# Performance work log

Hardware: AMD Instinct MI355X
Metric: run time of the kernel (lower is better)

## Reference

```python
import jax, jax.numpy as jnp
import numpy as np


def _bilinear_sample(tex, grid):
    """grid_sample, bilinear, align_corners=True, padding_mode='zeros'.
    tex: [C, Hin, Win]; grid: [B, Ho, Wo, 2] in [-1, 1] (x=width, y=height).
    Returns [B, C, Ho, Wo].
    """
    C, Hin, Win = tex.shape
    gx, gy = grid[..., 0], grid[..., 1]
    # align_corners=True mapping
    ix = (gx + 1.0) * 0.5 * (Win - 1)
    iy = (gy + 1.0) * 0.5 * (Hin - 1)
    ix0 = jnp.floor(ix)
    iy0 = jnp.floor(iy)
    wx1 = ix - ix0
    wy1 = iy - iy0
    wx0 = 1.0 - wx1
    wy0 = 1.0 - wy1

    def gather(iy_, ix_):
        valid = (ix_ >= 0) & (ix_ <= Win - 1) & (iy_ >= 0) & (iy_ <= Hin - 1)
        ic = jnp.clip(ix_, 0, Win - 1).astype(jnp.int32)
        jc = jnp.clip(iy_, 0, Hin - 1).astype(jnp.int32)
        v = tex[:, jc, ic]  # [C, B, Ho, Wo]
        return v * valid.astype(tex.dtype)[None]

    out = (gather(iy0, ix0) * (wy0 * wx0)[None]
           + gather(iy0, ix0 + 1) * (wy0 * wx1)[None]
           + gather(iy0 + 1, ix0) * (wy1 * wx0)[None]
           + gather(iy0 + 1, ix0 + 1) * (wy1 * wx1)[None])
    return jnp.transpose(out, (1, 0, 2, 3))  # [B, C, Ho, Wo]


def setup_inputs() -> dict:
    key = jax.random.key(0)
    k = jax.random.split(key, 6)
    B, C, W, H = 4, 16, 1024, 1024
    Ho, Wo = 512, 512
    return {
        "x": jax.random.uniform(k[0], (B, Ho, Wo, 2), dtype=jnp.float32),
        "x_msk": jax.random.uniform(k[1], (B, Ho, Wo), dtype=jnp.float32),
        "layer1": jax.random.normal(k[2], (C, W, H), dtype=jnp.float32),
        "layer2": jax.random.normal(k[3], (C, W // 2, H // 2), dtype=jnp.float32),
        "layer3": jax.random.normal(k[4], (C, W // 4, H // 4), dtype=jnp.float32),
        "layer4": jax.random.normal(k[5], (C, W // 8, H // 8), dtype=jnp.float32),
    }


def reference(x, x_msk, layer1, layer2, layer3, layer4):
    grid = x * 2.0 - 1.0
    y = (_bilinear_sample(layer1, grid)
         + _bilinear_sample(layer2, grid)
         + _bilinear_sample(layer3, grid)
         + _bilinear_sample(layer4, grid))
    return y * x_msk[:, None]
```

## Files before the change

kernel.cpp:

```cpp
#include <hip/hip_runtime.h>
#include <hip/hip_fp16.h>

#define CH 16
#define NPIX (4 * 512 * 512)
#define NBINS 4096
#define NBLK_SORT 256
#define PPB (NPIX / NBLK_SORT)
#define NILV 2720

typedef float vfloat4 __attribute__((ext_vector_type(4)));

__device__ __forceinline__ int bin_of(float xv, float yv) {
  int bx = min(max((int)(xv * 1023.0f), 0), 1023) >> 4;
  int by = min(max((int)(yv * 1023.0f), 0), 1023) >> 4;
  return (by << 6) + bx;
}

__global__ __launch_bounds__(256) void ilv_hist_kernel(
    const float* __restrict__ l1, const float* __restrict__ l2,
    const float* __restrict__ l3, const float* __restrict__ l4,
    __half* __restrict__ w1, __half* __restrict__ w2,
    __half* __restrict__ w3, __half* __restrict__ w4,
    const float2* __restrict__ x, unsigned* __restrict__ hist) {
  __shared__ unsigned s_lds[CH * 258];
  int b = blockIdx.x, t = threadIdx.x;
  if (b >= NILV) {
    int blk = b - NILV;
#pragma unroll
    for (int i = 0; i < NBINS / 256; ++i) s_lds[i * 256 + t] = 0;
    __syncthreads();
    int base = blk * PPB;
#pragma unroll 4
    for (int c = 0; c < PPB / 256; ++c) {
      float2 g = x[base + c * 256 + t];
      atomicAdd(&s_lds[bin_of(g.x, g.y)], 1u);
    }
    __syncthreads();
#pragma unroll
    for (int i = 0; i < NBINS / 256; ++i)
      hist[(size_t)blk * NBINS + i * 256 + t] = s_lds[i * 256 + t];
    return;
  }
  const float* src; __half* dst; int HW; size_t tb;
  if (b < 2048)      { src = l1; dst = w1; HW = 1048576; tb = (size_t)b * 512; }
  else if (b < 2560) { src = l2; dst = w2; HW = 262144;  tb = (size_t)(b - 2048) * 512; }
  else if (b < 2688) { src = l3; dst = w3; HW = 65536;   tb = (size_t)(b - 2560) * 512; }
  else               { src = l4; dst = w4; HW = 16384;   tb = (size_t)(b - 2688) * 512; }
  int lane = t & 63, cg = t >> 6;
#pragma unroll
  for (int j = 0; j < 4; ++j) {
    int c = cg * 4 + j;
    const vfloat4* s4 = (const vfloat4*)(src + (size_t)c * HW + tb);
#pragma unroll
    for (int half_ = 0; half_ < 2; ++half_) {
      vfloat4 v = __builtin_nontemporal_load(&s4[half_ * 64 + lane]);
      unsigned h0 = __half_as_ushort(__float2half(v.x));
      unsigned h1 = __half_as_ushort(__float2half(v.y));
      unsigned h2 = __half_as_ushort(__float2half(v.z));
      unsigned h3 = __half_as_ushort(__float2half(v.w));
      s_lds[c * 258 + half_ * 128 + lane * 2 + 0] = h0 | (h1 << 16);
      s_lds[c * 258 + half_ * 128 + lane * 2 + 1] = h2 | (h3 << 16);
    }
  }
  __syncthreads();
#pragma unroll
  for (int q = 0; q < 2; ++q) {
    int tt = t + q * 256;
    int idx = tt >> 1, sh = (tt & 1) * 16;
    unsigned o[8];
#pragma unroll
    for (int k = 0; k < 8; ++k) {
      unsigned lo = (s_lds[(2 * k + 0) * 258 + idx] >> sh) & 0xffffu;
      unsigned hi = (s_lds[(2 * k + 1) * 258 + idx] >> sh) & 0xffffu;
      o[k] = lo | (hi << 16);
    }
    uint4* d = (uint4*)(dst + (tb + tt) * CH);
    d[0] = make_uint4(o[0], o[1], o[2], o[3]);
    d[1] = make_uint4(o[4], o[5], o[6], o[7]);
  }
}

__global__ __launch_bounds__(256) void colscan2_kernel(
    unsigned* __restrict__ hist, unsigned* __restrict__ totals) {
  int bin = blockIdx.x * 256 + threadIdx.x;
  unsigned run = 0;
  for (int k = 0; k < NBLK_SORT; ++k) {
    size_t idx = (size_t)k * NBINS + bin;
    unsigned v = hist[idx];
    hist[idx] = run;
    run += v;
  }
  totals[bin] = run;
}

__global__ __launch_bounds__(1024) void scan_kernel(
    const unsigned* __restrict__ counts, unsigned* __restrict__ cursor) {
  __shared__ unsigned part[1024];
  int t = threadIdx.x;
  unsigned c0 = counts[4 * t + 0], c1 = counts[4 * t + 1];
  unsigned c2 = counts[4 * t + 2], c3 = counts[4 * t + 3];
  part[t] = c0 + c1 + c2 + c3;
  __syncthreads();
  for (int off = 1; off < 1024; off <<= 1) {
    unsigned v = (t >= off) ? part[t - off] : 0u;
    __syncthreads();
    part[t] += v;
    __syncthreads();
  }
  unsigned base = (t > 0) ? part[t - 1] : 0u;
  cursor[4 * t + 0] = base;
  cursor[4 * t + 1] = base + c0;
  cursor[4 * t + 2] = base + c0 + c1;
  cursor[4 * t + 3] = base + c0 + c1 + c2;
}

__global__ __launch_bounds__(256) void scatter2_kernel(
    const float2* __restrict__ x, const float* __restrict__ msk,
    const unsigned* __restrict__ hist, const unsigned* __restrict__ binbase,
    float4* __restrict__ pixrec) {
  __shared__ unsigned cur[NBINS];
  int tid = threadIdx.x, blk = blockIdx.x;
#pragma unroll
  for (int i = 0; i < NBINS / 256; ++i)
    cur[i * 256 + tid] = hist[(size_t)blk * NBINS + i * 256 + tid] +
                         binbase[i * 256 + tid];
  __syncthreads();
  int base = blk * PPB;
#pragma unroll 4
  for (int c = 0; c < PPB / 256; ++c) {
    int p = base + c * 256 + tid;
    float2 g = x[p];
    float m = msk[p];
    unsigned i = atomicAdd(&cur[bin_of(g.x, g.y)], 1u);
    pixrec[i] = make_float4(g.x, g.y, __uint_as_float((unsigned)p), m);
  }
}

__device__ __forceinline__ void sample_layer(const uint4* __restrict__ base,
                                             int W, float u, float v, int h,
                                             float c00, float c01, float c10,
                                             float c11, float acc[8]) {
  float ix = u * (float)(W - 1);
  float iy = v * (float)(W - 1);
  float fx = floorf(ix), fy = floorf(iy);
  float wx1 = ix - fx, wy1 = iy - fy;
  float wx0 = 1.0f - wx1, wy0 = 1.0f - wy1;
  int x0 = min(max((int)fx, 0), W - 1);
  int x1 = min(x0 + 1, W - 1);
  int y0 = min(max((int)fy, 0), W - 1);
  int y1 = min(y0 + 1, W - 1);
  union { uint4 u4; __half2 hh[4]; } a00, a01, a10, a11;
  a00.u4 = base[((size_t)y0 * W + x0) * 2 + h];
  a01.u4 = base[((size_t)y0 * W + x1) * 2 + h];
  a10.u4 = base[((size_t)y1 * W + x0) * 2 + h];
  a11.u4 = base[((size_t)y1 * W + x1) * 2 + h];
  __half2 w00h = __float2half2_rn(wy0 * wx0 * c00);
  __half2 w01h = __float2half2_rn(wy0 * wx1 * c01);
  __half2 w10h = __float2half2_rn(wy1 * wx0 * c10);
  __half2 w11h = __float2half2_rn(wy1 * wx1 * c11);
#pragma unroll
  for (int i = 0; i < 4; ++i) {
    __half2 s = __hmul2(a00.hh[i], w00h);
    s = __hfma2(a01.hh[i], w01h, s);
    s = __hfma2(a10.hh[i], w10h, s);
    s = __hfma2(a11.hh[i], w11h, s);
    float2 f = __half22float2(s);
    acc[2 * i + 0] += f.x;
    acc[2 * i + 1] += f.y;
  }
}

__global__ __launch_bounds__(256) void gather_binned4_kernel(
    const float4* __restrict__ pixrec,
    const __half* __restrict__ t1, const __half* __restrict__ t2,
    const __half* __restrict__ t3, const __half* __restrict__ t4,
    __half* __restrict__ ws2) {
  __shared__ float4 srec[128];
  __shared__ unsigned qcnt[16];
  __shared__ unsigned qb[16];
  __shared__ unsigned char perm[128];
  int tid = threadIdx.x;
  int bid = blockIdx.x;
  int swz = (bid & 7) * 1024 + (bid >> 3);
  int base = swz * 128;
  if (tid < 16) qcnt[tid] = 0;
  __syncthreads();
  unsigned key = 0, rank = 0;
  if ((tid & 1) == 0) {
    int pix = tid >> 1;
    float4 r = pixrec[base + pix];
    srec[pix] = r;
    int tx = min(max((int)(r.x * 1023.0f), 0), 1023);
    int ty = min(max((int)(r.y * 1023.0f), 0), 1023);
    key = ((((unsigned)ty >> 2) & 3u) << 2) | (((unsigned)tx >> 2) & 3u);
    rank = atomicAdd(&qcnt[key], 1u);
  }
  __syncthreads();
  if (tid == 0) {
    unsigned run = 0;
#pragma unroll
    for (int k = 0; k < 16; ++k) { qb[k] = run; run += qcnt[k]; }
  }
  __syncthreads();
  if ((tid & 1) == 0) perm[qb[key] + rank] = (unsigned char)(tid >> 1);
  __syncthreads();
  int j = tid >> 1;
  int h = tid & 1;
  float4 r = srec[perm[j]];
  float u = r.x, v = r.y;
  unsigned p = __float_as_uint(r.z);
  float m = r.w;
  float fx = floorf(u * 1023.0f), fy = floorf(v * 1023.0f);
  float vx0 = (fx >= 0.0f && fx <= 1023.0f) ? 1.0f : 0.0f;
  float vx1 = (fx + 1.0f >= 0.0f && fx + 1.0f <= 1023.0f) ? 1.0f : 0.0f;
  float vy0 = (fy >= 0.0f && fy <= 1023.0f) ? 1.0f : 0.0f;
  float vy1 = (fy + 1.0f >= 0.0f && fy + 1.0f <= 1023.0f) ? 1.0f : 0.0f;
  float c00 = vy0 * vx0, c01 = vy0 * vx1, c10 = vy1 * vx0, c11 = vy1 * vx1;
  float acc[8];
#pragma unroll
  for (int c = 0; c < 8; ++c) acc[c] = 0.0f;
  sample_layer((const uint4*)t1, 1024, u, v, h, c00, c01, c10, c11, acc);
  sample_layer((const uint4*)t2, 512, u, v, h, c00, c01, c10, c11, acc);
  sample_layer((const uint4*)t3, 256, u, v, h, c00, c01, c10, c11, acc);
  sample_layer((const uint4*)t4, 128, u, v, h, c00, c01, c10, c11, acc);
  union { __half2 hh[4]; uint4 u4; } o;
#pragma unroll
  for (int c = 0; c < 4; ++c)
    o.hh[c] = __floats2half2_rn(acc[2 * c] * m, acc[2 * c + 1] * m);
  ((uint4*)(ws2 + (size_t)p * CH))[h] = o.u4;
}

__global__ __launch_bounds__(256) void unscatter16_kernel(
    const __half* __restrict__ ws2, float* __restrict__ out) {
  int t = blockIdx.x * blockDim.x + threadIdx.x;
  int p0 = t * 4;
  int wo = p0 & 511, ho = (p0 >> 9) & 511, b = p0 >> 18;
  const uint4* s = (const uint4*)ws2;
  union { uint4 u[2]; __half2 h[8]; } v[4];
#pragma unroll
  for (int j = 0; j < 4; ++j) {
    v[j].u[0] = s[(size_t)(p0 + j) * 2 + 0];
    v[j].u[1] = s[(size_t)(p0 + j) * 2 + 1];
  }
  size_t obase = (size_t)b * (CH * 262144) + (size_t)ho * 512 + wo;
#pragma unroll
  for (int ch = 0; ch < CH; ++ch) {
    vfloat4 o;
    o.x = __half2float(((ch & 1) ? __high2half(v[0].h[ch >> 1]) : __low2half(v[0].h[ch >> 1])));
    o.y = __half2float(((ch & 1) ? __high2half(v[1].h[ch >> 1]) : __low2half(v[1].h[ch >> 1])));
    o.z = __half2float(((ch & 1) ? __high2half(v[2].h[ch >> 1]) : __low2half(v[2].h[ch >> 1])));
    o.w = __half2float(((ch & 1) ? __high2half(v[3].h[ch >> 1]) : __low2half(v[3].h[ch >> 1])));
    __builtin_nontemporal_store(o, (vfloat4*)(out + obase + (size_t)ch * 262144));
  }
}

__global__ __launch_bounds__(256) void interleave_lds2_kernel(
    const float* __restrict__ l1, const float* __restrict__ l2,
    const float* __restrict__ l3, const float* __restrict__ l4,
    __half* __restrict__ w1, __half* __restrict__ w2,
    __half* __restrict__ w3, __half* __restrict__ w4) {
  __shared__ unsigned lds_u[CH][258];
  int b = blockIdx.x;
  const float* src; __half* dst; int HW; size_t tb;
  if (b < 2048)      { src = l1; dst = w1; HW = 1048576; tb = (size_t)b * 512; }
  else if (b < 2560) { src = l2; dst = w2; HW = 262144;  tb = (size_t)(b - 2048) * 512; }
  else if (b < 2688) { src = l3; dst = w3; HW = 65536;   tb = (size_t)(b - 2560) * 512; }
  else               { src = l4; dst = w4; HW = 16384;   tb = (size_t)(b - 2688) * 512; }
  int t = threadIdx.x, lane = t & 63, cg = t >> 6;
#pragma unroll
  for (int j = 0; j < 4; ++j) {
    int c = cg * 4 + j;
    const vfloat4* s4 = (const vfloat4*)(src + (size_t)c * HW + tb);
#pragma unroll
    for (int half_ = 0; half_ < 2; ++half_) {
      vfloat4 v = __builtin_nontemporal_load(&s4[half_ * 64 + lane]);
      unsigned h0 = __half_as_ushort(__float2half(v.x));
      unsigned h1 = __half_as_ushort(__float2half(v.y));
      unsigned h2 = __half_as_ushort(__float2half(v.z));
      unsigned h3 = __half_as_ushort(__float2half(v.w));
      lds_u[c][half_ * 128 + lane * 2 + 0] = h0 | (h1 << 16);
      lds_u[c][half_ * 128 + lane * 2 + 1] = h2 | (h3 << 16);
    }
  }
  __syncthreads();
#pragma unroll
  for (int q = 0; q < 2; ++q) {
    int tt = t + q * 256;
    int idx = tt >> 1, sh = (tt & 1) * 16;
    unsigned o[8];
#pragma unroll
    for (int k = 0; k < 8; ++k) {
      unsigned lo = (lds_u[2 * k + 0][idx] >> sh) & 0xffffu;
      unsigned hi = (lds_u[2 * k + 1][idx] >> sh) & 0xffffu;
      o[k] = lo | (hi << 16);
    }
    uint4* d = (uint4*)(dst + (tb + tt) * CH);
    d[0] = make_uint4(o[0], o[1], o[2], o[3]);
    d[1] = make_uint4(o[4], o[5], o[6], o[7]);
  }
}

__device__ __forceinline__ void corner_fma(const __half* __restrict__ t,
                                           size_t texel, float w, float acc[CH]) {
  const uint4* q = (const uint4*)(t + texel * CH);
  union { uint4 u; __half2 h[4]; } a, b;
  a.u = q[0];
  b.u = q[1];
#pragma unroll
  for (int i = 0; i < 4; ++i) {
    float2 f = __half22float2(a.h[i]);
    acc[2 * i + 0] = fmaf(f.x, w, acc[2 * i + 0]);
    acc[2 * i + 1] = fmaf(f.y, w, acc[2 * i + 1]);
  }
#pragma unroll
  for (int i = 0; i < 4; ++i) {
    float2 f = __half22float2(b.h[i]);
    acc[8 + 2 * i + 0] = fmaf(f.x, w, acc[8 + 2 * i + 0]);
    acc[8 + 2 * i + 1] = fmaf(f.y, w, acc[8 + 2 * i + 1]);
  }
}

__device__ __forceinline__ void sample_hwc16(const __half* __restrict__ t, int W,
                                             float gx, float gy, float acc[CH]) {
  const float W1 = (float)(W - 1);
  float ix = (gx + 1.0f) * 0.5f * W1;
  float iy = (gy + 1.0f) * 0.5f * W1;
  float ix0f = floorf(ix), iy0f = floorf(iy);
  float wx1 = ix - ix0f, wy1 = iy - iy0f;
  float wx0 = 1.0f - wx1, wy0 = 1.0f - wy1;
  float ix1f = ix0f + 1.0f, iy1f = iy0f + 1.0f;
  float vx0 = (ix0f >= 0.0f && ix0f <= W1) ? 1.0f : 0.0f;
  float vx1 = (ix1f >= 0.0f && ix1f <= W1) ? 1.0f : 0.0f;
  float vy0 = (iy0f >= 0.0f && iy0f <= W1) ? 1.0f : 0.0f;
  float vy1 = (iy1f >= 0.0f && iy1f <= W1) ? 1.0f : 0.0f;
  int x0 = min(max((int)ix0f, 0), W - 1);
  int x1 = min(max((int)ix1f, 0), W - 1);
  int y0 = min(max((int)iy0f, 0), W - 1);
  int y1 = min(max((int)iy1f, 0), W - 1);
  float w00 = wy0 * wx0 * vy0 * vx0;
  float w01 = wy0 * wx1 * vy0 * vx1;
  float w10 = wy1 * wx0 * vy1 * vx0;
  float w11 = wy1 * wx1 * vy1 * vx1;
  corner_fma(t, (size_t)y0 * W + x0, w00, acc);
  corner_fma(t, (size_t)y0 * W + x1, w01, acc);
  corner_fma(t, (size_t)y1 * W + x0, w10, acc);
  corner_fma(t, (size_t)y1 * W + x1, w11, acc);
}

__global__ __launch_bounds__(256) void gather_hwc16_kernel(
    const float* __restrict__ x, const float* __restrict__ msk,
    const __half* __restrict__ t1, const __half* __restrict__ t2,
    const __half* __restrict__ t3, const __half* __restrict__ t4,
    float* __restrict__ out) {
  int p = blockIdx.x * blockDim.x + threadIdx.x;
  int wo = p & 511, ho = (p >> 9) & 511, b = p >> 18;
  float2 g = ((const float2*)x)[p];
  float gx = g.x * 2.0f - 1.0f;
  float gy = g.y * 2.0f - 1.0f;
  float m = msk[p];
  float acc[CH];
#pragma unroll
  for (int c = 0; c < CH; ++c) acc[c] = 0.0f;
  sample_hwc16(t1, 1024, gx, gy, acc);
  sample_hwc16(t2, 512, gx, gy, acc);
  sample_hwc16(t3, 256, gx, gy, acc);
  sample_hwc16(t4, 128, gx, gy, acc);
  size_t obase = (size_t)b * (CH * 262144) + (size_t)ho * 512 + wo;
#pragma unroll
  for (int c = 0; c < CH; ++c) out[obase + (size_t)c * 262144] = acc[c] * m;
}

__device__ __forceinline__ void sample_chw(const float* __restrict__ t, int W,
                                           float gx, float gy, float acc[CH]) {
  const float W1 = (float)(W - 1);
  float ix = (gx + 1.0f) * 0.5f * W1;
  float iy = (gy + 1.0f) * 0.5f * W1;
  float ix0f = floorf(ix), iy0f = floorf(iy);
  float wx1 = ix - ix0f, wy1 = iy - iy0f;
  float wx0 = 1.0f - wx1, wy0 = 1.0f - wy1;
  float ix1f = ix0f + 1.0f, iy1f = iy0f + 1.0f;
  float vx0 = (ix0f >= 0.0f && ix0f <= W1) ? 1.0f : 0.0f;
  float vx1 = (ix1f >= 0.0f && ix1f <= W1) ? 1.0f : 0.0f;
  float vy0 = (iy0f >= 0.0f && iy0f <= W1) ? 1.0f : 0.0f;
  float vy1 = (iy1f >= 0.0f && iy1f <= W1) ? 1.0f : 0.0f;
  int x0 = min(max((int)ix0f, 0), W - 1);
  int x1 = min(max((int)ix1f, 0), W - 1);
  int y0 = min(max((int)iy0f, 0), W - 1);
  int y1 = min(max((int)iy1f, 0), W - 1);
  float w00 = wy0 * wx0 * vy0 * vx0;
  float w01 = wy0 * wx1 * vy0 * vx1;
  float w10 = wy1 * wx0 * vy1 * vx0;
  float w11 = wy1 * wx1 * vy1 * vx1;
  size_t HW = (size_t)W * W;
  const float* b00 = t + (size_t)y0 * W + x0;
  const float* b01 = t + (size_t)y0 * W + x1;
  const float* b10 = t + (size_t)y1 * W + x0;
  const float* b11 = t + (size_t)y1 * W + x1;
#pragma unroll
  for (int c = 0; c < CH; ++c) {
    float v00 = b00[c * HW], v01 = b01[c * HW], v10 = b10[c * HW], v11 = b11[c * HW];
    acc[c] = fmaf(v00, w00, fmaf(v01, w01, fmaf(v10, w10, fmaf(v11, w11, acc[c]))));
  }
}

__global__ __launch_bounds__(256) void gather_chw_kernel(
    const float* __restrict__ x, const float* __restrict__ msk,
    const float* __restrict__ l1, const float* __restrict__ l2,
    const float* __restrict__ l3, const float* __restrict__ l4,
    float* __restrict__ out) {
  int p = blockIdx.x * blockDim.x + threadIdx.x;
  int wo = p & 511, ho = (p >> 9) & 511, b = p >> 18;
  float2 g = ((const float2*)x)[p];
  float gx = g.x * 2.0f - 1.0f;
  float gy = g.y * 2.0f - 1.0f;
  float m = msk[p];
  float acc[CH];
#pragma unroll
  for (int c = 0; c < CH; ++c) acc[c] = 0.0f;
  sample_chw(l1, 1024, gx, gy, acc);
  sample_chw(l2, 512, gx, gy, acc);
  sample_chw(l3, 256, gx, gy, acc);
  sample_chw(l4, 128, gx, gy, acc);
  size_t obase = (size_t)b * (CH * 262144) + (size_t)ho * 512 + wo;
#pragma unroll
  for (int c = 0; c < CH; ++c) out[obase + (size_t)c * 262144] = acc[c] * m;
}

extern "C" void kernel_launch(void* const* d_in, const int* in_sizes, int n_in,
                              void* d_out, int out_size, void* d_ws, size_t ws_size,
                              hipStream_t stream) {
  const float* x   = (const float*)d_in[0];
  const float* msk = (const float*)d_in[1];
  const float* l1  = (const float*)d_in[2];
  const float* l2  = (const float*)d_in[3];
  const float* l3  = (const float*)d_in[4];
  const float* l4  = (const float*)d_in[5];
  float* out = (float*)d_out;

  const size_t n_texel = 1048576 + 262144 + 65536 + 16384;
  const size_t tex_bytes = n_texel * CH * sizeof(__half);
  const size_t ws2_bytes = (size_t)NPIX * CH * sizeof(__half);
  const size_t rec_bytes = (size_t)NPIX * sizeof(float4);
  const size_t need_bin  = ws2_bytes + tex_bytes + rec_bytes;
  const size_t need_f16  = tex_bytes;

  if (ws_size >= need_bin) {
    char* base = (char*)d_ws;
    __half* ws2    = (__half*)base;
    __half* w1     = (__half*)(base + ws2_bytes);
    __half* w2     = w1 + (size_t)1048576 * CH;
    __half* w3     = w2 + (size_t)262144 * CH;
    __half* w4     = w3 + (size_t)65536 * CH;
    float4* pixrec = (float4*)(base + ws2_bytes + tex_bytes);
    unsigned* hist    = (unsigned*)base;
    unsigned* totals  = hist + (size_t)NBLK_SORT * NBINS;
    unsigned* binbase = totals + NBINS;

    ilv_hist_kernel<<<NILV + NBLK_SORT, 256, 0, stream>>>(
        l1, l2, l3, l4, w1, w2, w3, w4, (const float2*)x, hist);
    colscan2_kernel<<<NBINS / 256, 256, 0, stream>>>(hist, totals);
    scan_kernel<<<1, 1024, 0, stream>>>(totals, binbase);
    scatter2_kernel<<<NBLK_SORT, 256, 0, stream>>>(
        (const float2*)x, msk, hist, binbase, pixrec);
    gather_binned4_kernel<<<NPIX / 128, 256, 0, stream>>>(
        pixrec, w1, w2, w3, w4, ws2);
    unscatter16_kernel<<<NPIX / 4 / 256, 256, 0, stream>>>(ws2, out);
  } else if (ws_size >= need_f16) {
    __half* w1 = (__half*)d_ws;
    __half* w2 = w1 + (size_t)1048576 * CH;
    __half* w3 = w2 + (size_t)262144 * CH;
    __half* w4 = w3 + (size_t)65536 * CH;
    interleave_lds2_kernel<<<(int)(n_texel / 512), 256, 0, stream>>>(
        l1, l2, l3, l4, w1, w2, w3, w4);
    gather_hwc16_kernel<<<NPIX / 256, 256, 0, stream>>>(x, msk, w1, w2, w3, w4, out);
  } else {
    gather_chw_kernel<<<NPIX / 256, 256, 0, stream>>>(x, msk, l1, l2, l3, l4, out);
  }
}
```

Before: 108.0 us.

## Quantize pixel records to 16-bit coords, drop in-block sort, apply mask in unscatter

```diff
diff --git a/kernel.cpp b/kernel.cpp
--- a/kernel.cpp
+++ b/kernel.cpp
@@ -114,10 +114,9 @@
   cursor[4 * t + 3] = base + c0 + c1 + c2;
 }
 
-__global__ __launch_bounds__(256) void scatter2_kernel(
-    const float2* __restrict__ x, const float* __restrict__ msk,
-    const unsigned* __restrict__ hist, const unsigned* __restrict__ binbase,
-    float4* __restrict__ pixrec) {
+__global__ __launch_bounds__(256) void scatter3_kernel(
+    const float2* __restrict__ x, const unsigned* __restrict__ hist,
+    const unsigned* __restrict__ binbase, uint2* __restrict__ pixrec) {
   __shared__ unsigned cur[NBINS];
   int tid = threadIdx.x, blk = blockIdx.x;
 #pragma unroll
@@ -130,9 +129,10 @@
   for (int c = 0; c < PPB / 256; ++c) {
     int p = base + c * 256 + tid;
     float2 g = x[p];
-    float m = msk[p];
+    unsigned qu = min((unsigned)(g.x * 65536.0f), 65535u);
+    unsigned qv = min((unsigned)(g.y * 65536.0f), 65535u);
     unsigned i = atomicAdd(&cur[bin_of(g.x, g.y)], 1u);
-    pixrec[i] = make_float4(g.x, g.y, __uint_as_float((unsigned)p), m);
+    pixrec[i] = make_uint2((qv << 16) | qu, (unsigned)p);
   }
 }
 
@@ -170,46 +170,20 @@
   }
 }
 
-__global__ __launch_bounds__(256) void gather_binned4_kernel(
-    const float4* __restrict__ pixrec,
+__global__ __launch_bounds__(256) void gather_binned5_kernel(
+    const uint2* __restrict__ pixrec,
     const __half* __restrict__ t1, const __half* __restrict__ t2,
     const __half* __restrict__ t3, const __half* __restrict__ t4,
     __half* __restrict__ ws2) {
-  __shared__ float4 srec[128];
-  __shared__ unsigned qcnt[16];
-  __shared__ unsigned qb[16];
-  __shared__ unsigned char perm[128];
-  int tid = threadIdx.x;
   int bid = blockIdx.x;
   int swz = (bid & 7) * 1024 + (bid >> 3);
-  int base = swz * 128;
-  if (tid < 16) qcnt[tid] = 0;
-  __syncthreads();
-  unsigned key = 0, rank = 0;
-  if ((tid & 1) == 0) {
-    int pix = tid >> 1;
-    float4 r = pixrec[base + pix];
-    srec[pix] = r;
-    int tx = min(max((int)(r.x * 1023.0f), 0), 1023);
-    int ty = min(max((int)(r.y * 1023.0f), 0), 1023);
-    key = ((((unsigned)ty >> 2) & 3u) << 2) | (((unsigned)tx >> 2) & 3u);
-    rank = atomicAdd(&qcnt[key], 1u);
-  }
-  __syncthreads();
-  if (tid == 0) {
-    unsigned run = 0;
-#pragma unroll
-    for (int k = 0; k < 16; ++k) { qb[k] = run; run += qcnt[k]; }
-  }
-  __syncthreads();
-  if ((tid & 1) == 0) perm[qb[key] + rank] = (unsigned char)(tid >> 1);
-  __syncthreads();
-  int j = tid >> 1;
-  int h = tid & 1;
-  float4 r = srec[perm[j]];
-  float u = r.x, v = r.y;
-  unsigned p = __float_as_uint(r.z);
-  float m = r.w;
+  int g = swz * 256 + threadIdx.x;
+  int i = g >> 1;
+  int h = g & 1;
+  uint2 r = pixrec[i];
+  float u = ((float)(r.x & 0xffffu) + 0.5f) * (1.0f / 65536.0f);
+  float v = ((float)(r.x >> 16) + 0.5f) * (1.0f / 65536.0f);
+  unsigned p = r.y;
   float fx = floorf(u * 1023.0f), fy = floorf(v * 1023.0f);
   float vx0 = (fx >= 0.0f && fx <= 1023.0f) ? 1.0f : 0.0f;
   float vx1 = (fx + 1.0f >= 0.0f && fx + 1.0f <= 1023.0f) ? 1.0f : 0.0f;
@@ -226,15 +200,17 @@
   union { __half2 hh[4]; uint4 u4; } o;
 #pragma unroll
   for (int c = 0; c < 4; ++c)
-    o.hh[c] = __floats2half2_rn(acc[2 * c] * m, acc[2 * c + 1] * m);
+    o.hh[c] = __floats2half2_rn(acc[2 * c], acc[2 * c + 1]);
   ((uint4*)(ws2 + (size_t)p * CH))[h] = o.u4;
 }
 
-__global__ __launch_bounds__(256) void unscatter16_kernel(
-    const __half* __restrict__ ws2, float* __restrict__ out) {
+__global__ __launch_bounds__(256) void unscatter16m_kernel(
+    const __half* __restrict__ ws2, const float* __restrict__ msk,
+    float* __restrict__ out) {
   int t = blockIdx.x * blockDim.x + threadIdx.x;
   int p0 = t * 4;
   int wo = p0 & 511, ho = (p0 >> 9) & 511, b = p0 >> 18;
+  float4 m4 = ((const float4*)msk)[t];
   const uint4* s = (const uint4*)ws2;
   union { uint4 u[2]; __half2 h[8]; } v[4];
 #pragma unroll
@@ -246,10 +222,10 @@
 #pragma unroll
   for (int ch = 0; ch < CH; ++ch) {
     vfloat4 o;
-    o.x = __half2float(((ch & 1) ? __high2half(v[0].h[ch >> 1]) : __low2half(v[0].h[ch >> 1])));
-    o.y = __half2float(((ch & 1) ? __high2half(v[1].h[ch >> 1]) : __low2half(v[1].h[ch >> 1])));
-    o.z = __half2float(((ch & 1) ? __high2half(v[2].h[ch >> 1]) : __low2half(v[2].h[ch >> 1])));
-    o.w = __half2float(((ch & 1) ? __high2half(v[3].h[ch >> 1]) : __low2half(v[3].h[ch >> 1])));
+    o.x = __half2float(((ch & 1) ? __high2half(v[0].h[ch >> 1]) : __low2half(v[0].h[ch >> 1]))) * m4.x;
+    o.y = __half2float(((ch & 1) ? __high2half(v[1].h[ch >> 1]) : __low2half(v[1].h[ch >> 1]))) * m4.y;
+    o.z = __half2float(((ch & 1) ? __high2half(v[2].h[ch >> 1]) : __low2half(v[2].h[ch >> 1]))) * m4.z;
+    o.w = __half2float(((ch & 1) ? __high2half(v[3].h[ch >> 1]) : __low2half(v[3].h[ch >> 1]))) * m4.w;
     __builtin_nontemporal_store(o, (vfloat4*)(out + obase + (size_t)ch * 262144));
   }
 }
@@ -440,7 +416,7 @@
   const size_t n_texel = 1048576 + 262144 + 65536 + 16384;
   const size_t tex_bytes = n_texel * CH * sizeof(__half);
   const size_t ws2_bytes = (size_t)NPIX * CH * sizeof(__half);
-  const size_t rec_bytes = (size_t)NPIX * sizeof(float4);
+  const size_t rec_bytes = (size_t)NPIX * sizeof(uint2);
   const size_t need_bin  = ws2_bytes + tex_bytes + rec_bytes;
   const size_t need_f16  = tex_bytes;
 
@@ -451,7 +427,7 @@
     __half* w2     = w1 + (size_t)1048576 * CH;
     __half* w3     = w2 + (size_t)262144 * CH;
     __half* w4     = w3 + (size_t)65536 * CH;
-    float4* pixrec = (float4*)(base + ws2_bytes + tex_bytes);
+    uint2*  pixrec = (uint2*)(base + ws2_bytes + tex_bytes);
     unsigned* hist    = (unsigned*)base;
     unsigned* totals  = hist + (size_t)NBLK_SORT * NBINS;
     unsigned* binbase = totals + NBINS;
@@ -460,11 +436,11 @@
         l1, l2, l3, l4, w1, w2, w3, w4, (const float2*)x, hist);
     colscan2_kernel<<<NBINS / 256, 256, 0, stream>>>(hist, totals);
     scan_kernel<<<1, 1024, 0, stream>>>(totals, binbase);
-    scatter2_kernel<<<NBLK_SORT, 256, 0, stream>>>(
-        (const float2*)x, msk, hist, binbase, pixrec);
-    gather_binned4_kernel<<<NPIX / 128, 256, 0, stream>>>(
+    scatter3_kernel<<<NBLK_SORT, 256, 0, stream>>>(
+        (const float2*)x, hist, binbase, pixrec);
+    gather_binned5_kernel<<<NPIX * 2 / 256, 256, 0, stream>>>(
         pixrec, w1, w2, w3, w4, ws2);
-    unscatter16_kernel<<<NPIX / 4 / 256, 256, 0, stream>>>(ws2, out);
+    unscatter16m_kernel<<<NPIX / 4 / 256, 256, 0, stream>>>(ws2, msk, out);
   } else if (ws_size >= need_f16) {
     __half* w1 = (__half*)d_ws;
     __half* w2 = w1 + (size_t)1048576 * CH;
```

Measured after the change: 113.1 us. 1.05x slower.

## Hoist all texture loads in gather, drop in-block quad sort, reorder hist blocks

Applied to the files above, without the earlier changes.

```diff
diff --git a/kernel.cpp b/kernel.cpp
--- a/kernel.cpp
+++ b/kernel.cpp
@@ -23,9 +23,9 @@
     __half* __restrict__ w3, __half* __restrict__ w4,
     const float2* __restrict__ x, unsigned* __restrict__ hist) {
   __shared__ unsigned s_lds[CH * 258];
-  int b = blockIdx.x, t = threadIdx.x;
-  if (b >= NILV) {
-    int blk = b - NILV;
+  int b0 = blockIdx.x, t = threadIdx.x;
+  if (b0 < NBLK_SORT) {
+    int blk = b0;
 #pragma unroll
     for (int i = 0; i < NBINS / 256; ++i) s_lds[i * 256 + t] = 0;
     __syncthreads();
@@ -41,6 +41,7 @@
       hist[(size_t)blk * NBINS + i * 256 + t] = s_lds[i * 256 + t];
     return;
   }
+  int b = b0 - NBLK_SORT;
   const float* src; __half* dst; int HW; size_t tb;
   if (b < 2048)      { src = l1; dst = w1; HW = 1048576; tb = (size_t)b * 512; }
   else if (b < 2560) { src = l2; dst = w2; HW = 262144;  tb = (size_t)(b - 2048) * 512; }
@@ -136,93 +137,74 @@
   }
 }
 
-__device__ __forceinline__ void sample_layer(const uint4* __restrict__ base,
-                                             int W, float u, float v, int h,
-                                             float c00, float c01, float c10,
-                                             float c11, float acc[8]) {
-  float ix = u * (float)(W - 1);
-  float iy = v * (float)(W - 1);
-  float fx = floorf(ix), fy = floorf(iy);
-  float wx1 = ix - fx, wy1 = iy - fy;
-  float wx0 = 1.0f - wx1, wy0 = 1.0f - wy1;
-  int x0 = min(max((int)fx, 0), W - 1);
-  int x1 = min(x0 + 1, W - 1);
-  int y0 = min(max((int)fy, 0), W - 1);
-  int y1 = min(y0 + 1, W - 1);
-  union { uint4 u4; __half2 hh[4]; } a00, a01, a10, a11;
-  a00.u4 = base[((size_t)y0 * W + x0) * 2 + h];
-  a01.u4 = base[((size_t)y0 * W + x1) * 2 + h];
-  a10.u4 = base[((size_t)y1 * W + x0) * 2 + h];
-  a11.u4 = base[((size_t)y1 * W + x1) * 2 + h];
-  __half2 w00h = __float2half2_rn(wy0 * wx0 * c00);
-  __half2 w01h = __float2half2_rn(wy0 * wx1 * c01);
-  __half2 w10h = __float2half2_rn(wy1 * wx0 * c10);
-  __half2 w11h = __float2half2_rn(wy1 * wx1 * c11);
-#pragma unroll
-  for (int i = 0; i < 4; ++i) {
-    __half2 s = __hmul2(a00.hh[i], w00h);
-    s = __hfma2(a01.hh[i], w01h, s);
-    s = __hfma2(a10.hh[i], w10h, s);
-    s = __hfma2(a11.hh[i], w11h, s);
-    float2 f = __half22float2(s);
-    acc[2 * i + 0] += f.x;
-    acc[2 * i + 1] += f.y;
-  }
-}
-
-__global__ __launch_bounds__(256) void gather_binned4_kernel(
+__global__ __launch_bounds__(256) void gather_binned6_kernel(
     const float4* __restrict__ pixrec,
     const __half* __restrict__ t1, const __half* __restrict__ t2,
     const __half* __restrict__ t3, const __half* __restrict__ t4,
     __half* __restrict__ ws2) {
-  __shared__ float4 srec[128];
-  __shared__ unsigned qcnt[16];
-  __shared__ unsigned qb[16];
-  __shared__ unsigned char perm[128];
-  int tid = threadIdx.x;
   int bid = blockIdx.x;
   int swz = (bid & 7) * 1024 + (bid >> 3);
-  int base = swz * 128;
-  if (tid < 16) qcnt[tid] = 0;
-  __syncthreads();
-  unsigned key = 0, rank = 0;
-  if ((tid & 1) == 0) {
-    int pix = tid >> 1;
-    float4 r = pixrec[base + pix];
-    srec[pix] = r;
-    int tx = min(max((int)(r.x * 1023.0f), 0), 1023);
-    int ty = min(max((int)(r.y * 1023.0f), 0), 1023);
-    key = ((((unsigned)ty >> 2) & 3u) << 2) | (((unsigned)tx >> 2) & 3u);
-    rank = atomicAdd(&qcnt[key], 1u);
-  }
-  __syncthreads();
-  if (tid == 0) {
-    unsigned run = 0;
-#pragma unroll
-    for (int k = 0; k < 16; ++k) { qb[k] = run; run += qcnt[k]; }
-  }
-  __syncthreads();
-  if ((tid & 1) == 0) perm[qb[key] + rank] = (unsigned char)(tid >> 1);
-  __syncthreads();
-  int j = tid >> 1;
-  int h = tid & 1;
-  float4 r = srec[perm[j]];
+  int g = swz * 256 + threadIdx.x;
+  int i = g >> 1;
+  int h = g & 1;
+  float4 r = pixrec[i];
   float u = r.x, v = r.y;
   unsigned p = __float_as_uint(r.z);
   float m = r.w;
-  float fx = floorf(u * 1023.0f), fy = floorf(v * 1023.0f);
-  float vx0 = (fx >= 0.0f && fx <= 1023.0f) ? 1.0f : 0.0f;
-  float vx1 = (fx + 1.0f >= 0.0f && fx + 1.0f <= 1023.0f) ? 1.0f : 0.0f;
-  float vy0 = (fy >= 0.0f && fy <= 1023.0f) ? 1.0f : 0.0f;
-  float vy1 = (fy + 1.0f >= 0.0f && fy + 1.0f <= 1023.0f) ? 1.0f : 0.0f;
+  float fx1 = floorf(u * 1023.0f), fy1 = floorf(v * 1023.0f);
+  float vx0 = (fx1 >= 0.0f && fx1 <= 1023.0f) ? 1.0f : 0.0f;
+  float vx1 = (fx1 + 1.0f >= 0.0f && fx1 + 1.0f <= 1023.0f) ? 1.0f : 0.0f;
+  float vy0 = (fy1 >= 0.0f && fy1 <= 1023.0f) ? 1.0f : 0.0f;
+  float vy1 = (fy1 + 1.0f >= 0.0f && fy1 + 1.0f <= 1023.0f) ? 1.0f : 0.0f;
   float c00 = vy0 * vx0, c01 = vy0 * vx1, c10 = vy1 * vx0, c11 = vy1 * vx1;
+
+  const uint4* T[4] = {(const uint4*)t1, (const uint4*)t2,
+                       (const uint4*)t3, (const uint4*)t4};
+  const int Ws[4] = {1024, 512, 256, 128};
+  uint4 A[4][4];
+  float wx1s[4], wy1s[4];
+#pragma unroll
+  for (int L = 0; L < 4; ++L) {
+    int W = Ws[L];
+    float ix = u * (float)(W - 1);
+    float iy = v * (float)(W - 1);
+    float fx = floorf(ix), fy = floorf(iy);
+    wx1s[L] = ix - fx;
+    wy1s[L] = iy - fy;
+    int x0 = min(max((int)fx, 0), W - 1);
+    int x1 = min(x0 + 1, W - 1);
+    int y0 = min(max((int)fy, 0), W - 1);
+    int y1 = min(y0 + 1, W - 1);
+    const uint4* base = T[L];
+    A[L][0] = base[((size_t)y0 * W + x0) * 2 + h];
+    A[L][1] = base[((size_t)y0 * W + x1) * 2 + h];
+    A[L][2] = base[((size_t)y1 * W + x0) * 2 + h];
+    A[L][3] = base[((size_t)y1 * W + x1) * 2 + h];
+  }
   float acc[8];
 #pragma unroll
   for (int c = 0; c < 8; ++c) acc[c] = 0.0f;
-  sample_layer((const uint4*)t1, 1024, u, v, h, c00, c01, c10, c11, acc);
-  sample_layer((const uint4*)t2, 512, u, v, h, c00, c01, c10, c11, acc);
-  sample_layer((const uint4*)t3, 256, u, v, h, c00, c01, c10, c11, acc);
-  sample_layer((const uint4*)t4, 128, u, v, h, c00, c01, c10, c11, acc);
+#pragma unroll
+  for (int L = 0; L < 4; ++L) {
+    float wx1 = wx1s[L], wy1 = wy1s[L];
+    float wx0 = 1.0f - wx1, wy0 = 1.0f - wy1;
+    __half2 w00h = __float2half2_rn(wy0 * wx0 * c00);
+    __half2 w01h = __float2half2_rn(wy0 * wx1 * c01);
+    __half2 w10h = __float2half2_rn(wy1 * wx0 * c10);
+    __half2 w11h = __float2half2_rn(wy1 * wx1 * c11);
+    union { uint4 u4; __half2 hh[4]; } a00, a01, a10, a11;
+    a00.u4 = A[L][0]; a01.u4 = A[L][1]; a10.u4 = A[L][2]; a11.u4 = A[L][3];
+#pragma unroll
+    for (int k = 0; k < 4; ++k) {
+      __half2 s = __hmul2(a00.hh[k], w00h);
+      s = __hfma2(a01.hh[k], w01h, s);
+      s = __hfma2(a10.hh[k], w10h, s);
+      s = __hfma2(a11.hh[k], w11h, s);
+      float2 f = __half22float2(s);
+      acc[2 * k + 0] += f.x;
+      acc[2 * k + 1] += f.y;
+    }
+  }
   union { __half2 hh[4]; uint4 u4; } o;
 #pragma unroll
   for (int c = 0; c < 4; ++c)
@@ -462,7 +444,7 @@
     scan_kernel<<<1, 1024, 0, stream>>>(totals, binbase);
     scatter2_kernel<<<NBLK_SORT, 256, 0, stream>>>(
         (const float2*)x, msk, hist, binbase, pixrec);
-    gather_binned4_kernel<<<NPIX / 128, 256, 0, stream>>>(
+    gather_binned6_kernel<<<NPIX * 2 / 256, 256, 0, stream>>>(
         pixrec, w1, w2, w3, w4, ws2);
     unscatter16_kernel<<<NPIX / 4 / 256, 256, 0, stream>>>(ws2, out);
   } else if (ws_size >= need_f16) {
```

Result: no change. 107.7 us (-0.3%).
